# Performance work log

Hardware: AMD Instinct MI355X
Metric: run time of the kernel (lower is better)

## Reference

```python
import jax, jax.numpy as jnp
import numpy as np

LOCAL_RANGE = 2
STRIDE = 2
NEG = 1e10

def stride_sparse_mask(N):
    i = np.arange(N)[:, None]
    j = np.arange(N)[None, :]
    d = np.abs(j - i)
    return ((d <= LOCAL_RANGE) | (d % STRIDE == 0)).astype(np.float32)

def setup_inputs() -> dict:
    key = jax.random.key(0)
    k1, k2, k3, k4 = jax.random.split(key, 4)
    B, S, D, H = 4, 2048, 512, 8
    # glorot-uniform-like scale for (D, D) weight slices
    lim = np.sqrt(6.0 / (D + D)).astype(np.float32)
    inputs = jax.random.normal(k1, (B, 1, S, D), dtype=jnp.float32)
    Wq = jax.random.uniform(k2, (H, D, D), minval=-lim, maxval=lim, dtype=jnp.float32)
    Wk = jax.random.uniform(k3, (H, D, D), minval=-lim, maxval=lim, dtype=jnp.float32)
    Wv = jax.random.uniform(k4, (H, D, D), minval=-lim, maxval=lim, dtype=jnp.float32)
    return {"inputs": inputs, "Wq": Wq, "Wk": Wk, "Wv": Wv}

def reference(inputs, Wq, Wk, Wv):
    # inputs: (B, 1, S, D); Wq/Wk/Wv: (H, D, D)
    B, _, S, D = inputs.shape
    H = Wq.shape[0]
    x = inputs[:, 0]  # (B, S, D)
    mask = jnp.asarray(stride_sparse_mask(S))  # (S, S), static
    # Batched over heads: equivalent to the original per-head Python loop.
    Q = jnp.einsum('bsd,hdk->bhsk', x, Wq)
    K = jnp.einsum('bsd,hdk->bhsk', x, Wk)
    V = jnp.einsum('bsd,hdk->bhsk', x, Wv)
    scores = jnp.einsum('bhsk,bhtk->bhst', Q, K) / jnp.sqrt(jnp.float32(D))
    # Original applies the 0/1 mask once (head 0) or twice (later heads);
    # double application is mathematically identical to a single one.
    scores = scores * mask - NEG * (1.0 - mask)
    attn = jax.nn.softmax(scores, axis=-1)
    out = jnp.einsum('bhst,bhtk->bhsk', attn, V)  # (B, H, S, D)
    total = jnp.mean(out, axis=1)  # average over heads
    return total[:, None, :, :]  # (B, 1, S, D)
```

## Files before the change

kernel.cpp:

```cpp
#include <hip/hip_runtime.h>
#include <stdint.h>

#define Bdim 4
#define Sdim 2048
#define Ddim 512
#define Hdim 8
#define Mdim (Bdim*Sdim)
#define Shalf 1024

typedef __attribute__((ext_vector_type(8))) short bf16x8;
typedef __attribute__((ext_vector_type(4))) float f32x4;
typedef __attribute__((ext_vector_type(16))) float f32x16;
typedef __attribute__((ext_vector_type(4))) int i32x4;

#define SCALE 0.044194173824159216f
#define LOG2E 1.4426950408889634f

__device__ __forceinline__ unsigned short f2bf(float f){
  union { float f; unsigned int u; } v; v.f = f;
  unsigned int u = v.u + 0x7FFFu + ((v.u >> 16) & 1u);
  return (unsigned short)(u >> 16);
}

__device__ __forceinline__ void gl_lds16(const void* g, void* l){
  __builtin_amdgcn_global_load_lds(
      (const __attribute__((address_space(1))) unsigned int*)g,
      (__attribute__((address_space(3))) unsigned int*)l, 16, 0, 0);
}

__device__ __forceinline__ int permrow(int m){
  return (m & ~2047) | ((m & 1) << 10) | ((m & 2047) >> 1);
}

__global__ void cvt_x(const float* __restrict__ x, unsigned short* __restrict__ xb, int n8){
  int i = blockIdx.x*blockDim.x + threadIdx.x;
  if (i >= n8) return;
  const float4* p = (const float4*)x + (size_t)i*2;
  float4 a = p[0], b = p[1];
  union { unsigned short s[8]; i32x4 v; } o;
  o.s[0]=f2bf(a.x); o.s[1]=f2bf(a.y); o.s[2]=f2bf(a.z); o.s[3]=f2bf(a.w);
  o.s[4]=f2bf(b.x); o.s[5]=f2bf(b.y); o.s[6]=f2bf(b.z); o.s[7]=f2bf(b.w);
  ((i32x4*)xb)[i] = o.v;
}

__global__ void twk(const float* __restrict__ Wq, const float* __restrict__ Wk,
                    const float* __restrict__ Wv, unsigned short* __restrict__ Wt){
  __shared__ float t[32][33];
  int z = blockIdx.z;
  const float* W = (z < Hdim ? Wq : (z < 2*Hdim ? Wk : Wv)) + (size_t)(z % Hdim)*Ddim*Ddim;
  int n0 = blockIdx.x*32, k0 = blockIdx.y*32;
  #pragma unroll
  for (int i=0;i<4;i++){
    int k = k0 + threadIdx.y + i*8;
    t[threadIdx.y + i*8][threadIdx.x] = W[(size_t)k*Ddim + n0 + threadIdx.x];
  }
  __syncthreads();
  #pragma unroll
  for (int i=0;i<4;i++){
    int n = threadIdx.y + i*8;
    Wt[(size_t)z*Ddim*Ddim + (size_t)(n0+n)*Ddim + k0 + threadIdx.x] = f2bf(t[threadIdx.x][n]);
  }
}

__launch_bounds__(256, 2)
__global__ void proj(const unsigned short* __restrict__ xb,
                     const unsigned short* __restrict__ Wt,
                     unsigned short* __restrict__ Qb,
                     unsigned short* __restrict__ Kb,
                     unsigned short* __restrict__ Vtb,
                     int h0, int g)
{
  __shared__ unsigned short smem[16640];
  int tid = threadIdx.x, w = tid>>6, lane = tid&63;
  int wm = w>>1, wn = w&1;
  int y = blockIdx.y, g4 = 4*g;
  int type = y / g4; int rem = y - type*g4;
  int hrel = rem >> 2, nt = rem & 3;
  int m0 = blockIdx.x * 128, n0 = nt * 128;
  int l15 = lane&15, l4 = lane>>4;

  const unsigned short* Bsrc = Wt + (size_t)(type*Hdim + h0 + hrel)*Ddim*Ddim;

  f32x4 acc[4][4];
  #pragma unroll
  for (int i=0;i<4;i++)
    #pragma unroll
    for (int j=0;j<4;j++){ f32x4 z={0.f,0.f,0.f,0.f}; acc[i][j]=z; }

  for (int kt=0; kt<16; ++kt){
    int k0 = kt*32;
    #pragma unroll
    for (int i=0;i<2;i++){
      int row = i*64 + w*16 + (lane>>2);
      int cb  = lane&3;
      gl_lds16(xb   + (size_t)(m0+row)*Ddim + k0 + cb*8, (char*)smem + i*4096 + w*1024);
      gl_lds16(Bsrc + (size_t)(n0+row)*Ddim + k0 + cb*8, (char*)smem + 8192 + i*4096 + w*1024);
    }
    __syncthreads();
    bf16x8 af[4], bfr[4];
    #pragma unroll
    for (int i=0;i<4;i++){
      af[i]  = *(const bf16x8*)&smem[(wm*64 + i*16 + l15)*32 + l4*8];
      bfr[i] = *(const bf16x8*)&smem[4096 + (wn*64 + i*16 + l15)*32 + l4*8];
    }
    #pragma unroll
    for (int i=0;i<4;i++)
      #pragma unroll
      for (int j=0;j<4;j++)
        acc[i][j] = __builtin_amdgcn_mfma_f32_16x16x32_bf16(af[i], bfr[j], acc[i][j], 0,0,0);
    __syncthreads();
  }

  if (type < 2){
    unsigned short* Ob = (type==0 ? Qb : Kb) + (size_t)hrel*Mdim*Ddim;
    #pragma unroll
    for (int i=0;i<4;i++){
      int mb = m0 + wm*64 + i*16 + (l4<<2);
      #pragma unroll
      for (int j=0;j<4;j++){
        int col = n0 + wn*64 + j*16 + l15;
        #pragma unroll
        for (int r=0;r<4;r++)
          Ob[(size_t)permrow(mb + r)*Ddim + col] = f2bf(acc[i][j][r]);
      }
    }
  } else {
    #pragma unroll
    for (int i=0;i<4;i++){
      int ml = wm*64 + i*16 + (l4<<2);
      #pragma unroll
      for (int j=0;j<4;j++){
        int nl = wn*64 + j*16 + l15;
        #pragma unroll
        for (int r=0;r<4;r++)
          smem[(ml + r)*130 + nl] = f2bf(acc[i][j][r]);
      }
    }
    __syncthreads();
    unsigned short* Ovt = Vtb + (size_t)hrel*Ddim*Mdim;
    int bb  = m0 >> 11;
    int ib0 = (m0 & 2047) >> 1;
    #pragma unroll
    for (int c=0;c<8;c++){
      int nl = c*16 + (tid>>4);
      int il = (tid&15)*4;
      #pragma unroll
      for (int pp=0; pp<2; pp++){
        union { unsigned short s[4]; uint2 v; } pk;
        #pragma unroll
        for (int ii=0;ii<4;ii++) pk.s[ii] = smem[(2*(il+ii)+pp)*130 + nl];
        *(uint2*)&Ovt[(size_t)(n0+nl)*Mdim + bb*Sdim + pp*Shalf + ib0 + il] = pk.v;
      }
    }
  }
}

__device__ __forceinline__ void stage_dense(const unsigned short* Kbase, int krow0,
                                            const unsigned short* Vblk, int vcol0,
                                            char* KsB, char* VsB, int w, int lane)
{
  int l15 = lane&15, l4 = lane>>4;
  #pragma unroll
  for (int jj=0;jj<4;jj++){
    int bi = w*4 + jj;
    int row = krow0 + ((bi>>4)<<4) + l15;
    int g   = ((bi&15)<<2) + l4;
    gl_lds16(Kbase + ((size_t)row<<9) + g*8, KsB + bi*1024);
    int d   = (bi<<4) + l15;
    int col = vcol0 + l4*8;
    gl_lds16(Vblk + ((size_t)d<<13) + col, VsB + bi*1024);
  }
}
__device__ __forceinline__ void stage_spec(const unsigned short* Kbase, int krow0,
                                           const unsigned short* Vblk, int vcol0,
                                           char* KsB, char* VsB, int w, int lane)
{
  int l15 = lane&15, l4 = lane>>4;
  #pragma unroll
  for (int jj=0;jj<4;jj++){
    int bi = w*4 + jj;
    int row = krow0 + ((bi>>4)<<4) + l15;
    row = row < 0 ? 0 : (row > Shalf-1 ? Shalf-1 : row);
    int g   = ((bi&15)<<2) + l4;
    gl_lds16(Kbase + ((size_t)row<<9) + g*8, KsB + bi*1024);
    int d   = (bi<<4) + l15;
    int col = vcol0 + l4*8;
    col = col < 0 ? 0 : (col > Shalf-8 ? Shalf-8 : col);
    gl_lds16(Vblk + ((size_t)d<<13) + col, VsB + bi*1024);
  }
}

#define NDENSE 32
#define NSPEC 5
#define NT (NDENSE + NSPEC)

__launch_bounds__(512, 2)
__global__ void attn(const unsigned short* __restrict__ Qb,
                     const unsigned short* __restrict__ Kb,
                     const unsigned short* __restrict__ Vtb,
                     float* __restrict__ out)
{
  __shared__ char lds[163840];
  int tid = threadIdx.x, w = tid>>6, lane = tid&63;
  int qg = w>>1, dg = w&1;
  int ql = lane&31, hh = lane>>5;
  int z  = blockIdx.x;
  int qc = blockIdx.y;
  int p  = z & 1; int zb = z >> 1; int b = zb & 3; int hd = zb >> 2;

  const unsigned short* Qp    = Qb + (size_t)hd*Mdim*Ddim + (size_t)(b*Sdim + p*Shalf)*Ddim;
  const unsigned short* Ksame = Kb + (size_t)hd*Mdim*Ddim + (size_t)(b*Sdim + p*Shalf)*Ddim;
  const unsigned short* Kopp  = Kb + (size_t)hd*Mdim*Ddim + (size_t)(b*Sdim + (1-p)*Shalf)*Ddim;
  const unsigned short* Vt    = Vtb + (size_t)hd*Ddim*Mdim;
  int csame = b*Sdim + p*Shalf;
  int copp  = b*Sdim + (1-p)*Shalf;
  int i0 = qc*128;
  int j0 = i0 - 32 + 32*p;

  const float C1 = SCALE*LOG2E;
  const float C0 = -4.0f*LOG2E;

  bf16x8 qf[16];
  {
    const unsigned short* qr = Qp + (size_t)(i0 + qg*32 + ql)*Ddim + dg*256 + hh*8;
    #pragma unroll
    for (int st=0; st<16; ++st) qf[st] = *(const bf16x8*)(qr + st*16);
  }

  f32x16 acc[8];
  #pragma unroll
  for (int dt=0; dt<8; ++dt)
    #pragma unroll
    for (int j=0; j<16; ++j) acc[dt][j] = 0.f;
  float lpp[4] = {0.f, 0.f, 0.f, 0.f};

  char* Kbuf = lds;
  char* Xch  = lds + 131072;
  int iq  = i0 + qg*32 + ql;
  int tgt = iq - 1 + 2*p;

  stage_dense(Ksame, 0, Vt + csame, 0, Kbuf, lds + 32768, w, lane);

  int vb = 0;
  for (int t=0; t<NT; ++t){
    char* VsB = lds + 32768 + vb*32768;

    asm volatile("s_waitcnt vmcnt(0)" ::: "memory");
    __builtin_amdgcn_s_barrier();
    __builtin_amdgcn_sched_barrier(0);

    f32x16 sc;
    #pragma unroll
    for (int j=0; j<16; ++j) sc[j] = 0.f;
    #pragma unroll
    for (int st=0; st<16; ++st){
      int c = dg*32 + st*2 + hh;
      bf16x8 kf = *(const bf16x8*)(Kbuf + ((ql>>4)*16 + (c>>2))*1024 + (c&3)*256 + (ql&15)*16);
      sc = __builtin_amdgcn_mfma_f32_32x32x16_bf16(kf, qf[st], sc, 0,0,0);
    }

    char* Xw = Xch + w*4096;
    #pragma unroll
    for (int i=0;i<4;i++){
      f32x4 v;
      #pragma unroll
      for (int j=0;j<4;j++) v[j] = sc[4*i+j];
      *(f32x4*)(Xw + i*1024 + lane*16) = v;
    }
    asm volatile("s_waitcnt lgkmcnt(0)" ::: "memory");
    __builtin_amdgcn_sched_barrier(0);
    __builtin_amdgcn_s_barrier();
    __builtin_amdgcn_sched_barrier(0);

    int vbn = vb + 1; if (vbn == 3) vbn = 0;
    if (t + 1 < NT){
      char* VsN = lds + 32768 + vbn*32768;
      if (t + 1 < NDENSE)
        stage_dense(Ksame, (t+1)*32, Vt + csame, (t+1)*32, Kbuf, VsN, w, lane);
      else {
        int tt = t + 1 - NDENSE;
        stage_spec(Kopp, j0 + tt*32, Vt + copp, j0 + tt*32, Kbuf, VsN, w, lane);
      }
    }

    char* Xp = Xch + (w^1)*4096;
    float pr[16];
    bool spec = (t >= NDENSE);
    int tbase = spec ? (j0 + (t-NDENSE)*32) : 0;
    #pragma unroll
    for (int i=0;i<4;i++){
      f32x4 v = *(const f32x4*)(Xp + i*1024 + lane*16);
      #pragma unroll
      for (int j=0;j<4;j++){
        int r = 4*i+j;
        float s = sc[r] + v[j];
        float pe = exp2f(s*C1 + C0);
        if (spec){
          int jk = tbase + (r&3) + 8*(r>>2) + 4*hh;
          bool ok = (jk>=0) & (jk<Shalf) & ((jk==iq) | (jk==tgt));
          pe = ok ? pe : 0.f;
        }
        pr[r] = pe;
        lpp[i] += pe;
      }
    }

    union { unsigned int u[4]; bf16x8 v; } pa0, pa1;
    {
      unsigned int X, Y;
      asm("v_cvt_pk_bf16_f32 %0, %1, %2" : "=v"(X) : "v"(pr[0]),  "v"(pr[1]));
      asm("v_cvt_pk_bf16_f32 %0, %1, %2" : "=v"(Y) : "v"(pr[4]),  "v"(pr[5]));
      asm("v_permlane32_swap_b32 %0, %1" : "+v"(X), "+v"(Y));
      pa0.u[0] = X; pa0.u[2] = Y;
      asm("v_cvt_pk_bf16_f32 %0, %1, %2" : "=v"(X) : "v"(pr[2]),  "v"(pr[3]));
      asm("v_cvt_pk_bf16_f32 %0, %1, %2" : "=v"(Y) : "v"(pr[6]),  "v"(pr[7]));
      asm("v_permlane32_swap_b32 %0, %1" : "+v"(X), "+v"(Y));
      pa0.u[1] = X; pa0.u[3] = Y;
      asm("v_cvt_pk_bf16_f32 %0, %1, %2" : "=v"(X) : "v"(pr[8]),  "v"(pr[9]));
      asm("v_cvt_pk_bf16_f32 %0, %1, %2" : "=v"(Y) : "v"(pr[12]), "v"(pr[13]));
      asm("v_permlane32_swap_b32 %0, %1" : "+v"(X), "+v"(Y));
      pa1.u[0] = X; pa1.u[2] = Y;
      asm("v_cvt_pk_bf16_f32 %0, %1, %2" : "=v"(X) : "v"(pr[10]), "v"(pr[11]));
      asm("v_cvt_pk_bf16_f32 %0, %1, %2" : "=v"(Y) : "v"(pr[14]), "v"(pr[15]));
      asm("v_permlane32_swap_b32 %0, %1" : "+v"(X), "+v"(Y));
      pa1.u[1] = X; pa1.u[3] = Y;
    }

    #pragma unroll
    for (int dt=0; dt<8; ++dt){
      int bi = dg*16 + dt*2 + ((lane>>4)&1);
      bf16x8 vf0 = *(const bf16x8*)(VsB + bi*1024 + hh*256 + (lane&15)*16);
      acc[dt] = __builtin_amdgcn_mfma_f32_32x32x16_bf16(pa0.v, vf0, acc[dt], 0,0,0);
      bf16x8 vf1 = *(const bf16x8*)(VsB + bi*1024 + (2+hh)*256 + (lane&15)*16);
      acc[dt] = __builtin_amdgcn_mfma_f32_32x32x16_bf16(pa1.v, vf1, acc[dt], 0,0,0);
    }
    vb = vbn;
  }

  float lp = (lpp[0] + lpp[1]) + (lpp[2] + lpp[3]);
  float lpq = lp + __shfl_xor(lp, 32);
  #pragma unroll
  for (int r=0;r<16;++r){
    int qrow = (r&3) + 8*(r>>2) + 4*hh;
    float inv = 0.125f / __shfl(lpq, qrow);
    int orow = b*Sdim + 2*(i0 + qg*32 + qrow) + p;
    float* op = out + (size_t)orow*Ddim + dg*256 + ql;
    #pragma unroll
    for (int dt=0; dt<8; ++dt)
      atomicAdd(op + dt*32, acc[dt][r]*inv);
  }
}

extern "C" void kernel_launch(void* const* d_in, const int* in_sizes, int n_in,
                              void* d_out, int out_size, void* d_ws, size_t ws_size,
                              hipStream_t stream)
{
  (void)in_sizes; (void)n_in;
  const float* x  = (const float*)d_in[0];
  const float* Wq = (const float*)d_in[1];
  const float* Wk = (const float*)d_in[2];
  const float* Wv = (const float*)d_in[3];
  float* out = (float*)d_out;

  const size_t xb_bytes = (size_t)Mdim*Ddim*2;
  const size_t wt_bytes = (size_t)3*Hdim*Ddim*Ddim*2;
  const size_t per_head = (size_t)Mdim*Ddim*2;

  int g = 8;
  while (g > 1 && xb_bytes + wt_bytes + 3*(size_t)g*per_head > ws_size) g >>= 1;

  unsigned short* xb  = (unsigned short*)d_ws;
  unsigned short* Wt  = (unsigned short*)((char*)d_ws + xb_bytes);
  unsigned short* Qb  = (unsigned short*)((char*)d_ws + xb_bytes + wt_bytes);
  unsigned short* Kb  = Qb + (size_t)g*Mdim*Ddim;
  unsigned short* Vtb = Kb + (size_t)g*Mdim*Ddim;

  hipMemsetAsync(d_out, 0, (size_t)out_size*sizeof(float), stream);
  cvt_x<<<dim3(Mdim*Ddim/8/256), dim3(256), 0, stream>>>(x, xb, Mdim*Ddim/8);
  twk<<<dim3(Ddim/32, Ddim/32, 3*Hdim), dim3(32,8), 0, stream>>>(Wq, Wk, Wv, Wt);

  for (int h0 = 0; h0 < Hdim; h0 += g){
    proj<<<dim3(Mdim/128, 12*g), dim3(256), 0, stream>>>(xb, Wt, Qb, Kb, Vtb, h0, g);
    attn<<<dim3(g*Bdim*2, Shalf/128 ), dim3(512), 0, stream>>>(Qb, Kb, Vtb, out);
  }
}
```

Baseline: 487.3 us.

## Split attention head dimension across four waves and double-buffer V staging

The attention kernel now runs 1024 threads per block. Each of four waves per query group handles a quarter of the 512-wide head dimension, so each wave keeps half as many Q fragments and output accumulators, and partial scores are summed across four exchange slots. V tiles are double-buffered and prefetched at the top of each iteration, while K staging is issued after the score phase. The aim is to raise the number of resident waves and hide load latency, at the cost of more LDS exchange traffic and more barrier participants per block.

```diff
diff --git a/kernel.cpp b/kernel.cpp
--- a/kernel.cpp
+++ b/kernel.cpp
@@ -155,38 +155,30 @@
   }
 }
 
-__device__ __forceinline__ void stage_dense(const unsigned short* Kbase, int krow0,
-                                            const unsigned short* Vblk, int vcol0,
-                                            char* KsB, char* VsB, int w, int lane)
+__device__ __forceinline__ void stage_v16(const unsigned short* Vblk, int vcol0,
+                                          char* VsB, int w, int lane, bool clamp)
 {
   int l15 = lane&15, l4 = lane>>4;
   #pragma unroll
-  for (int jj=0;jj<4;jj++){
-    int bi = w*4 + jj;
+  for (int jj=0;jj<2;jj++){
+    int bi = w*2 + jj;
+    int d   = (bi<<4) + l15;
+    int col = vcol0 + l4*8;
+    if (clamp) col = col < 0 ? 0 : (col > Shalf-8 ? Shalf-8 : col);
+    gl_lds16(Vblk + ((size_t)d<<13) + col, VsB + bi*1024);
+  }
+}
+__device__ __forceinline__ void stage_k16(const unsigned short* Kbase, int krow0,
+                                          char* KsB, int w, int lane, bool clamp)
+{
+  int l15 = lane&15, l4 = lane>>4;
+  #pragma unroll
+  for (int jj=0;jj<2;jj++){
+    int bi = w*2 + jj;
     int row = krow0 + ((bi>>4)<<4) + l15;
+    if (clamp) row = row < 0 ? 0 : (row > Shalf-1 ? Shalf-1 : row);
     int g   = ((bi&15)<<2) + l4;
     gl_lds16(Kbase + ((size_t)row<<9) + g*8, KsB + bi*1024);
-    int d   = (bi<<4) + l15;
-    int col = vcol0 + l4*8;
-    gl_lds16(Vblk + ((size_t)d<<13) + col, VsB + bi*1024);
-  }
-}
-__device__ __forceinline__ void stage_spec(const unsigned short* Kbase, int krow0,
-                                           const unsigned short* Vblk, int vcol0,
-                                           char* KsB, char* VsB, int w, int lane)
-{
-  int l15 = lane&15, l4 = lane>>4;
-  #pragma unroll
-  for (int jj=0;jj<4;jj++){
-    int bi = w*4 + jj;
-    int row = krow0 + ((bi>>4)<<4) + l15;
-    row = row < 0 ? 0 : (row > Shalf-1 ? Shalf-1 : row);
-    int g   = ((bi&15)<<2) + l4;
-    gl_lds16(Kbase + ((size_t)row<<9) + g*8, KsB + bi*1024);
-    int d   = (bi<<4) + l15;
-    int col = vcol0 + l4*8;
-    col = col < 0 ? 0 : (col > Shalf-8 ? Shalf-8 : col);
-    gl_lds16(Vblk + ((size_t)d<<13) + col, VsB + bi*1024);
   }
 }
 
@@ -194,7 +186,7 @@
 #define NSPEC 5
 #define NT (NDENSE + NSPEC)
 
-__launch_bounds__(512, 2)
+__launch_bounds__(1024, 4)
 __global__ void attn(const unsigned short* __restrict__ Qb,
                      const unsigned short* __restrict__ Kb,
                      const unsigned short* __restrict__ Vtb,
@@ -202,7 +194,7 @@
 {
   __shared__ char lds[163840];
   int tid = threadIdx.x, w = tid>>6, lane = tid&63;
-  int qg = w>>1, dg = w&1;
+  int qg = w>>2, dg = w&3;
   int ql = lane&31, hh = lane>>5;
   int z  = blockIdx.x;
   int qc = blockIdx.y;
@@ -220,133 +212,135 @@
   const float C1 = SCALE*LOG2E;
   const float C0 = -4.0f*LOG2E;
 
-  bf16x8 qf[16];
+  bf16x8 qf[8];
   {
-    const unsigned short* qr = Qp + (size_t)(i0 + qg*32 + ql)*Ddim + dg*256 + hh*8;
-    #pragma unroll
-    for (int st=0; st<16; ++st) qf[st] = *(const bf16x8*)(qr + st*16);
-  }
-
-  f32x16 acc[8];
-  #pragma unroll
-  for (int dt=0; dt<8; ++dt)
+    const unsigned short* qr = Qp + (size_t)(i0 + qg*32 + ql)*Ddim + dg*128 + hh*8;
+    #pragma unroll
+    for (int st=0; st<8; ++st) qf[st] = *(const bf16x8*)(qr + st*16);
+  }
+
+  f32x16 acc[4];
+  #pragma unroll
+  for (int dt=0; dt<4; ++dt)
     #pragma unroll
     for (int j=0; j<16; ++j) acc[dt][j] = 0.f;
-  float lpp[4] = {0.f, 0.f, 0.f, 0.f};
+  float lpp[2] = {0.f, 0.f};
 
   char* Kbuf = lds;
-  char* Xch  = lds + 131072;
+  char* Xch  = lds + 98304;
+  char* XwB  = Xch + w*4096;
+  char* Xp0  = Xch + (qg*4 + ((dg+1)&3))*4096;
+  char* Xp1  = Xch + (qg*4 + ((dg+2)&3))*4096;
+  char* Xp2  = Xch + (qg*4 + ((dg+3)&3))*4096;
   int iq  = i0 + qg*32 + ql;
   int tgt = iq - 1 + 2*p;
 
-  stage_dense(Ksame, 0, Vt + csame, 0, Kbuf, lds + 32768, w, lane);
-
-  int vb = 0;
+  stage_k16(Ksame, 0, Kbuf, w, lane, false);
+  stage_v16(Vt + csame, 0, lds + 32768, w, lane, false);
+
   for (int t=0; t<NT; ++t){
-    char* VsB = lds + 32768 + vb*32768;
+    char* VsB = lds + 32768 + (t&1)*32768;
 
     asm volatile("s_waitcnt vmcnt(0)" ::: "memory");
     __builtin_amdgcn_s_barrier();
     __builtin_amdgcn_sched_barrier(0);
 
+    if (t + 1 < NT){
+      char* VsN = lds + 32768 + ((t+1)&1)*32768;
+      if (t + 1 < NDENSE) stage_v16(Vt + csame, (t+1)*32, VsN, w, lane, false);
+      else                stage_v16(Vt + copp,  j0 + (t+1-NDENSE)*32, VsN, w, lane, true);
+    }
+
     f32x16 sc;
     #pragma unroll
     for (int j=0; j<16; ++j) sc[j] = 0.f;
     #pragma unroll
-    for (int st=0; st<16; ++st){
-      int c = dg*32 + st*2 + hh;
+    for (int st=0; st<8; ++st){
+      int c = dg*16 + st*2 + hh;
       bf16x8 kf = *(const bf16x8*)(Kbuf + ((ql>>4)*16 + (c>>2))*1024 + (c&3)*256 + (ql&15)*16);
       sc = __builtin_amdgcn_mfma_f32_32x32x16_bf16(kf, qf[st], sc, 0,0,0);
     }
 
-    char* Xw = Xch + w*4096;
     #pragma unroll
     for (int i=0;i<4;i++){
       f32x4 v;
       #pragma unroll
       for (int j=0;j<4;j++) v[j] = sc[4*i+j];
-      *(f32x4*)(Xw + i*1024 + lane*16) = v;
+      *(f32x4*)(XwB + i*1024 + lane*16) = v;
     }
     asm volatile("s_waitcnt lgkmcnt(0)" ::: "memory");
     __builtin_amdgcn_sched_barrier(0);
     __builtin_amdgcn_s_barrier();
     __builtin_amdgcn_sched_barrier(0);
 
-    int vbn = vb + 1; if (vbn == 3) vbn = 0;
     if (t + 1 < NT){
-      char* VsN = lds + 32768 + vbn*32768;
-      if (t + 1 < NDENSE)
-        stage_dense(Ksame, (t+1)*32, Vt + csame, (t+1)*32, Kbuf, VsN, w, lane);
-      else {
-        int tt = t + 1 - NDENSE;
-        stage_spec(Kopp, j0 + tt*32, Vt + copp, j0 + tt*32, Kbuf, VsN, w, lane);
-      }
-    }
-
-    char* Xp = Xch + (w^1)*4096;
-    float pr[16];
+      if (t + 1 < NDENSE) stage_k16(Ksame, (t+1)*32, Kbuf, w, lane, false);
+      else                stage_k16(Kopp,  j0 + (t+1-NDENSE)*32, Kbuf, w, lane, true);
+    }
+
     bool spec = (t >= NDENSE);
     int tbase = spec ? (j0 + (t-NDENSE)*32) : 0;
     #pragma unroll
     for (int i=0;i<4;i++){
-      f32x4 v = *(const f32x4*)(Xp + i*1024 + lane*16);
+      f32x4 v0 = *(const f32x4*)(Xp0 + i*1024 + lane*16);
+      f32x4 v1 = *(const f32x4*)(Xp1 + i*1024 + lane*16);
+      f32x4 v2 = *(const f32x4*)(Xp2 + i*1024 + lane*16);
       #pragma unroll
       for (int j=0;j<4;j++){
         int r = 4*i+j;
-        float s = sc[r] + v[j];
+        float s = (sc[r] + v0[j]) + (v1[j] + v2[j]);
         float pe = exp2f(s*C1 + C0);
         if (spec){
           int jk = tbase + (r&3) + 8*(r>>2) + 4*hh;
           bool ok = (jk>=0) & (jk<Shalf) & ((jk==iq) | (jk==tgt));
           pe = ok ? pe : 0.f;
         }
-        pr[r] = pe;
-        lpp[i] += pe;
+        sc[r] = pe;
+        lpp[i&1] += pe;
       }
     }
 
     union { unsigned int u[4]; bf16x8 v; } pa0, pa1;
     {
       unsigned int X, Y;
-      asm("v_cvt_pk_bf16_f32 %0, %1, %2" : "=v"(X) : "v"(pr[0]),  "v"(pr[1]));
-      asm("v_cvt_pk_bf16_f32 %0, %1, %2" : "=v"(Y) : "v"(pr[4]),  "v"(pr[5]));
+      asm("v_cvt_pk_bf16_f32 %0, %1, %2" : "=v"(X) : "v"(sc[0]),  "v"(sc[1]));
+      asm("v_cvt_pk_bf16_f32 %0, %1, %2" : "=v"(Y) : "v"(sc[4]),  "v"(sc[5]));
       asm("v_permlane32_swap_b32 %0, %1" : "+v"(X), "+v"(Y));
       pa0.u[0] = X; pa0.u[2] = Y;
-      asm("v_cvt_pk_bf16_f32 %0, %1, %2" : "=v"(X) : "v"(pr[2]),  "v"(pr[3]));
-      asm("v_cvt_pk_bf16_f32 %0, %1, %2" : "=v"(Y) : "v"(pr[6]),  "v"(pr[7]));
+      asm("v_cvt_pk_bf16_f32 %0, %1, %2" : "=v"(X) : "v"(sc[2]),  "v"(sc[3]));
+      asm("v_cvt_pk_bf16_f32 %0, %1, %2" : "=v"(Y) : "v"(sc[6]),  "v"(sc[7]));
       asm("v_permlane32_swap_b32 %0, %1" : "+v"(X), "+v"(Y));
       pa0.u[1] = X; pa0.u[3] = Y;
-      asm("v_cvt_pk_bf16_f32 %0, %1, %2" : "=v"(X) : "v"(pr[8]),  "v"(pr[9]));
-      asm("v_cvt_pk_bf16_f32 %0, %1, %2" : "=v"(Y) : "v"(pr[12]), "v"(pr[13]));
+      asm("v_cvt_pk_bf16_f32 %0, %1, %2" : "=v"(X) : "v"(sc[8]),  "v"(sc[9]));
+      asm("v_cvt_pk_bf16_f32 %0, %1, %2" : "=v"(Y) : "v"(sc[12]), "v"(sc[13]));
       asm("v_permlane32_swap_b32 %0, %1" : "+v"(X), "+v"(Y));
       pa1.u[0] = X; pa1.u[2] = Y;
-      asm("v_cvt_pk_bf16_f32 %0, %1, %2" : "=v"(X) : "v"(pr[10]), "v"(pr[11]));
-      asm("v_cvt_pk_bf16_f32 %0, %1, %2" : "=v"(Y) : "v"(pr[14]), "v"(pr[15]));
+      asm("v_cvt_pk_bf16_f32 %0, %1, %2" : "=v"(X) : "v"(sc[10]), "v"(sc[11]));
+      asm("v_cvt_pk_bf16_f32 %0, %1, %2" : "=v"(Y) : "v"(sc[14]), "v"(sc[15]));
       asm("v_permlane32_swap_b32 %0, %1" : "+v"(X), "+v"(Y));
       pa1.u[1] = X; pa1.u[3] = Y;
     }
 
     #pragma unroll
-    for (int dt=0; dt<8; ++dt){
-      int bi = dg*16 + dt*2 + ((lane>>4)&1);
+    for (int dt=0; dt<4; ++dt){
+      int bi = dg*8 + dt*2 + ((lane>>4)&1);
       bf16x8 vf0 = *(const bf16x8*)(VsB + bi*1024 + hh*256 + (lane&15)*16);
       acc[dt] = __builtin_amdgcn_mfma_f32_32x32x16_bf16(pa0.v, vf0, acc[dt], 0,0,0);
       bf16x8 vf1 = *(const bf16x8*)(VsB + bi*1024 + (2+hh)*256 + (lane&15)*16);
       acc[dt] = __builtin_amdgcn_mfma_f32_32x32x16_bf16(pa1.v, vf1, acc[dt], 0,0,0);
     }
-    vb = vbn;
-  }
-
-  float lp = (lpp[0] + lpp[1]) + (lpp[2] + lpp[3]);
+  }
+
+  float lp = lpp[0] + lpp[1];
   float lpq = lp + __shfl_xor(lp, 32);
   #pragma unroll
   for (int r=0;r<16;++r){
     int qrow = (r&3) + 8*(r>>2) + 4*hh;
     float inv = 0.125f / __shfl(lpq, qrow);
     int orow = b*Sdim + 2*(i0 + qg*32 + qrow) + p;
-    float* op = out + (size_t)orow*Ddim + dg*256 + ql;
-    #pragma unroll
-    for (int dt=0; dt<8; ++dt)
+    float* op = out + (size_t)orow*Ddim + dg*128 + ql;
+    #pragma unroll
+    for (int dt=0; dt<4; ++dt)
       atomicAdd(op + dt*32, acc[dt][r]*inv);
   }
 }
@@ -381,6 +375,6 @@
 
   for (int h0 = 0; h0 < Hdim; h0 += g){
     proj<<<dim3(Mdim/128, 12*g), dim3(256), 0, stream>>>(xb, Wt, Qb, Kb, Vtb, h0, g);
-    attn<<<dim3(g*Bdim*2, Shalf/128 ), dim3(512), 0, stream>>>(Qb, Kb, Vtb, out);
-  }
-}
+    attn<<<dim3(g*Bdim*2, Shalf/128 ), dim3(1024), 0, stream>>>(Qb, Kb, Vtb, out);
+  }
+}
```

Result: slower. 807.5 us (+65.7%).
